# Kernel tuning notes

Measured on AMD Instinct MI355X. Metric: run time of the kernel, lower is better.

The kernel has to match this reference:

```python
import jax, jax.numpy as jnp
import numpy as np

HEAD = 16
NEG = -1.0e9


def setup_inputs() -> dict:
    key = jax.random.key(0)
    ks = jax.random.split(key, 8)
    B, S, D = 2, 2048, 1024
    scale = 1.0 / np.sqrt(D)
    inp = {
        "query": jax.random.normal(ks[0], (B, S, D), jnp.float32),
        "key": jax.random.normal(ks[1], (B, S, D), jnp.float32),
        "value": jax.random.normal(ks[2], (B, S, D), jnp.float32),
        "mask": jnp.ones((B, S, S), jnp.int32),
        "w_q": jax.random.normal(ks[3], (D, D), jnp.float32) * scale,
        "b_q": jnp.zeros((D,), jnp.float32),
        "w_k": jax.random.normal(ks[4], (D, D), jnp.float32) * scale,
        "b_k": jnp.zeros((D,), jnp.float32),
        "w_v": jax.random.normal(ks[5], (D, D), jnp.float32) * scale,
        "b_v": jnp.zeros((D,), jnp.float32),
        "w_o": jax.random.normal(ks[6], (D, D), jnp.float32) * scale,
        "b_o": jnp.zeros((D,), jnp.float32),
    }
    return inp


def _split_heads(x, B, S, H, dk):
    # [B,S,D] -> [B,H,S,dk]
    return x.reshape(B, S, H, dk).transpose(0, 2, 1, 3)


def reference(query, key, value, mask, w_q, b_q, w_k, b_k, w_v, b_v, w_o, b_o):
    B, S, D = query.shape
    H = HEAD
    dk = D // H
    q = _split_heads(query @ w_q.T + b_q, B, S, H, dk)
    k = _split_heads(key @ w_k.T + b_k, B, S, H, dk)
    v = _split_heads(value @ w_v.T + b_v, B, S, H, dk)
    # scores: [B,H,S,S]
    scores = jnp.einsum('bhqd,bhkd->bhqk', q, k) / jnp.sqrt(jnp.float32(dk))
    scores = jnp.where(mask[:, None, :, :] == 0, NEG, scores)
    p = jax.nn.softmax(scores, axis=-1)  # dropout is identity in eval
    x = jnp.einsum('bhqk,bhkd->bhqd', p, v)  # [B,H,S,dk]
    x = x.transpose(0, 2, 1, 3).reshape(B, S, D)
    return x @ w_o.T + b_o
```

## Files before the change

kernel.cpp:

```cpp
#include <hip/hip_runtime.h>

typedef float f32x4 __attribute__((ext_vector_type(4)));
typedef short bf16x8 __attribute__((ext_vector_type(8)));
typedef unsigned short u16x4 __attribute__((ext_vector_type(4)));

#define BB 2
#define SS 2048
#define DM 1024
#define NH 16
#define DKH 64
#define MROWS 4096

__device__ __forceinline__ unsigned short f2bf(float x) {
  union { float f; unsigned int u; } v; v.f = x;
  unsigned int r = v.u + 0x7fffu + ((v.u >> 16) & 1u);
  return (unsigned short)(r >> 16);
}

__device__ __forceinline__ void gll16(const void* g, void* l) {
  __builtin_amdgcn_global_load_lds(
      (const __attribute__((address_space(1))) void*)g,
      (__attribute__((address_space(3))) void*)l, 16, 0, 0);
}

template <int C>
__device__ __forceinline__ float dppf(float x) {
  return __builtin_bit_cast(float,
      __builtin_amdgcn_mov_dpp(__builtin_bit_cast(int, x), C, 0xf, 0xf, true));
}
__device__ __forceinline__ float rowmax16(float v) {
  v = fmaxf(v, dppf<0xB1>(v));
  v = fmaxf(v, dppf<0x4E>(v));
  v = fmaxf(v, dppf<0x141>(v));
  v = fmaxf(v, dppf<0x140>(v));
  return v;
}
__device__ __forceinline__ float rowsum16(float v) {
  v += dppf<0xB1>(v);
  v += dppf<0x4E>(v);
  v += dppf<0x141>(v);
  v += dppf<0x140>(v);
  return v;
}

struct CvtArgs {
  const float* src[7];
  unsigned short* dst[7];
  int n4[7];
};

__global__ __launch_bounds__(256) void cvt7_kernel(CvtArgs a) {
  const int z = blockIdx.y;
  const int i = blockIdx.x * 256 + threadIdx.x;
  if (i >= a.n4[z]) return;
  f32x4 v = ((const f32x4*)a.src[z])[i];
  u16x4 o;
  o[0] = f2bf(v[0]); o[1] = f2bf(v[1]); o[2] = f2bf(v[2]); o[3] = f2bf(v[3]);
  ((u16x4*)a.dst[z])[i] = o;
}

__global__ __launch_bounds__(256) void mask_flags_kernel(const int* __restrict__ mask,
                                                         int* __restrict__ flags) {
  const int bid = blockIdx.x;
  const int b = bid >> 9, qt = (bid >> 4) & 31, kt = bid & 15;
  __shared__ int sf;
  if (threadIdx.x == 0) sf = 0;
  __syncthreads();
  int any0 = 0;
  const size_t base = ((size_t)b * SS + qt * 64) * SS + kt * 128;
  for (int p = 0; p < 32; ++p) {
    int i = p * 256 + threadIdx.x;
    int r = i >> 7, col = i & 127;
    any0 |= (mask[base + (size_t)r * SS + col] == 0);
  }
  if (any0) sf = 1;
  __syncthreads();
  if (threadIdx.x == 0) flags[bid] = sf;
}

struct ProjArgs {
  const unsigned short* A[3];
  const unsigned short* W[3];
  const float* bias[3];
  void* out[3];
  float alpha[3];
  int mode[3];
};

__global__ __launch_bounds__(256, 2) void proj_gemm(ProjArgs args) {
  __shared__ unsigned short As[128][32];
  __shared__ unsigned short Bs[128][32];
  const int z = blockIdx.z;
  const unsigned short* __restrict__ A = args.A[z];
  const unsigned short* __restrict__ W = args.W[z];
  const float* __restrict__ bias = args.bias[z];
  const float alpha = args.alpha[z];
  const int mode = args.mode[z];

  const int tid = threadIdx.x;
  const int w = tid >> 6, lane = tid & 63;
  const int quad = lane >> 4, c = lane & 15;
  const int m0 = blockIdx.x * 128, n0 = blockIdx.y * 128;
  const int wm = (w >> 1) * 64, wn = (w & 1) * 64;
  const int sr = lane >> 2, scc = lane & 3;
  const int lx = scc ^ ((sr >> 1) & 3);
  const int sk = (quad ^ ((c >> 1) & 3)) * 8;

  f32x4 acc[4][4];
#pragma unroll
  for (int i = 0; i < 4; ++i)
#pragma unroll
    for (int j = 0; j < 4; ++j) { f32x4 zz = {0.f, 0.f, 0.f, 0.f}; acc[i][j] = zz; }

  for (int kt = 0; kt < 32; ++kt) {
    const int k0 = kt * 32;
    __syncthreads();
#pragma unroll
    for (int t = 0; t < 2; ++t) {
      const int tt = w + t * 4;
      const int r = tt * 16 + sr;
      gll16(A + (size_t)(m0 + r) * DM + k0 + lx * 8, &As[r][scc * 8]);
      gll16(W + (size_t)(n0 + r) * DM + k0 + lx * 8, &Bs[r][scc * 8]);
    }
    __syncthreads();
    bf16x8 af[4], bfr[4];
#pragma unroll
    for (int i = 0; i < 4; ++i) af[i] = *(const bf16x8*)&As[wm + i * 16 + c][sk];
#pragma unroll
    for (int j = 0; j < 4; ++j) bfr[j] = *(const bf16x8*)&Bs[wn + j * 16 + c][sk];
#pragma unroll
    for (int i = 0; i < 4; ++i)
#pragma unroll
      for (int j = 0; j < 4; ++j)
        acc[i][j] = __builtin_amdgcn_mfma_f32_16x16x32_bf16(af[i], bfr[j], acc[i][j], 0, 0, 0);
  }

#pragma unroll
  for (int i = 0; i < 4; ++i)
#pragma unroll
    for (int j = 0; j < 4; ++j)
#pragma unroll
      for (int r = 0; r < 4; ++r) {
        const int m = m0 + wm + i * 16 + quad * 4 + r;
        const int n = n0 + wn + j * 16 + c;
        const float val = (acc[i][j][r] + bias[n]) * alpha;
        if (mode == 2) {
          ((float*)args.out[z])[(size_t)m * DM + n] = val;
        } else {
          const int bb = m >> 11, s = m & 2047, hh = n >> 6, d = n & 63;
          size_t idx;
          if (mode == 0) {
            idx = (((size_t)(bb * NH + hh)) * SS + s) * DKH + d;
          } else {
            const int sl = s & 127, blk = s >> 7;
            const int jj = sl >> 4, rem = sl & 15, kc = rem >> 2, qd = rem & 3;
            const int pos = kc * 32 + qd * 8 + jj;
            idx = (((size_t)(bb * NH + hh)) * DKH + d) * SS + blk * 128 + pos;
          }
          ((unsigned short*)args.out[z])[idx] = f2bf(val);
        }
      }
}

__global__ __launch_bounds__(256, 3) void attn_kernel(
    const unsigned short* __restrict__ qp, const unsigned short* __restrict__ kp,
    const unsigned short* __restrict__ vtp, const int* __restrict__ mask,
    const int* __restrict__ flags, unsigned short* __restrict__ xb) {
  __shared__ __align__(16) char smem[50176];
  unsigned short (*Ks)[128][32] = (unsigned short (*)[128][32])smem;
  unsigned short (*Vt)[64][32]  = (unsigned short (*)[64][32])(smem + 16384);
  unsigned short (*Qs)[64][32]  = (unsigned short (*)[64][32])(smem + 32768);
  unsigned short (*Ps)[136]     = (unsigned short (*)[136])(smem + 32768);

  const int tid = threadIdx.x;
  const int w = tid >> 6, lane = tid & 63;
  const int quad = lane >> 4, c = lane & 15;
  const int qt = blockIdx.x, bh = blockIdx.y;
  const int b = bh >> 4, h = bh & 15;
  const int q0 = qt * 64;
  const int sr = lane >> 2, scc = lane & 3;
  const int lx = scc ^ ((sr >> 1) & 3);
  const int sk = (quad ^ ((c >> 1) & 3)) * 8;

#pragma unroll
  for (int t = 0; t < 2; ++t) {
    const int tt = w + t * 4;
    const int kk = tt >> 2;
    const int r = (tt & 3) * 16 + sr;
    gll16(qp + ((size_t)bh * SS + q0 + r) * DKH + kk * 32 + lx * 8, &Qs[kk][r][scc * 8]);
  }
  __syncthreads();
  const bf16x8 aq0 = *(const bf16x8*)&Qs[0][w * 16 + c][sk];
  const bf16x8 aq1 = *(const bf16x8*)&Qs[1][w * 16 + c][sk];

  f32x4 acco[4];
#pragma unroll
  for (int j = 0; j < 4; ++j) { f32x4 zz = {0.f, 0.f, 0.f, 0.f}; acco[j] = zz; }
  float m_run[4], l_run[4];
#pragma unroll
  for (int r = 0; r < 4; ++r) { m_run[r] = -3.0e38f; l_run[r] = 0.f; }

  for (int kt = 0; kt < 16; ++kt) {
    const int k0 = kt * 128;
    __syncthreads();
#pragma unroll
    for (int i = 0; i < 4; ++i) {
      const int tt = w * 4 + i;
      {
        const int kk = tt >> 3, r = (tt & 7) * 16 + sr;
        gll16(kp + ((size_t)bh * SS + k0 + r) * DKH + kk * 32 + lx * 8, &Ks[kk][r][scc * 8]);
      }
      {
        const int kc = tt >> 2, d = (tt & 3) * 16 + sr;
        gll16(vtp + ((size_t)bh * DKH + d) * SS + k0 + kc * 32 + lx * 8, &Vt[kc][d][scc * 8]);
      }
    }
    __syncthreads();

    f32x4 accs[8];
#pragma unroll
    for (int j = 0; j < 8; ++j) { f32x4 zz = {0.f, 0.f, 0.f, 0.f}; accs[j] = zz; }
#pragma unroll
    for (int j = 0; j < 8; ++j) {
      const int rowk = j * 16 + c;
      const bf16x8 bk0 = *(const bf16x8*)&Ks[0][rowk][sk];
      const bf16x8 bk1 = *(const bf16x8*)&Ks[1][rowk][sk];
      accs[j] = __builtin_amdgcn_mfma_f32_16x16x32_bf16(aq0, bk0, accs[j], 0, 0, 0);
      accs[j] = __builtin_amdgcn_mfma_f32_16x16x32_bf16(aq1, bk1, accs[j], 0, 0, 0);
    }

    if (flags[((size_t)b * 32 + qt) * 16 + kt]) {
#pragma unroll
      for (int j = 0; j < 8; ++j)
#pragma unroll
        for (int r = 0; r < 4; ++r) {
          const int qq = q0 + w * 16 + quad * 4 + r;
          const int kk2 = k0 + j * 16 + c;
          if (mask[((size_t)b * SS + qq) * SS + kk2] == 0) accs[j][r] = -1.0e30f;
        }
    }

    float al[4];
#pragma unroll
    for (int r = 0; r < 4; ++r) {
      float v = accs[0][r];
#pragma unroll
      for (int j = 1; j < 8; ++j) v = fmaxf(v, accs[j][r]);
      v = rowmax16(v);
      const float mn = fmaxf(m_run[r], v);
      al[r] = __builtin_amdgcn_exp2f(m_run[r] - mn);
      m_run[r] = mn;
      float s = 0.f;
      union { bf16x8 v8; unsigned short u[8]; } pk;
#pragma unroll
      for (int j = 0; j < 8; ++j) {
        const float p = __builtin_amdgcn_exp2f(accs[j][r] - mn);
        union { float f; unsigned int u; } pv; pv.f = p;
        pk.u[j] = (unsigned short)(pv.u >> 16);
        union { unsigned int u; float f; } pr; pr.u = pv.u & 0xffff0000u;
        s += pr.f;
      }
      *(bf16x8*)&Ps[w * 16 + quad * 4 + r][c * 8] = pk.v8;
      s = rowsum16(s);
      l_run[r] = l_run[r] * al[r] + s;
    }
#pragma unroll
    for (int j = 0; j < 4; ++j)
#pragma unroll
      for (int r = 0; r < 4; ++r) acco[j][r] *= al[r];

#pragma unroll
    for (int kc = 0; kc < 4; ++kc) {
      const bf16x8 ap = *(const bf16x8*)&Ps[w * 16 + c][kc * 32 + quad * 8];
#pragma unroll
      for (int j = 0; j < 4; ++j) {
        const bf16x8 bv = *(const bf16x8*)&Vt[kc][j * 16 + c][sk];
        acco[j] = __builtin_amdgcn_mfma_f32_16x16x32_bf16(ap, bv, acco[j], 0, 0, 0);
      }
    }
  }

#pragma unroll
  for (int r = 0; r < 4; ++r) {
    const float inv = 1.0f / l_run[r];
    const int q = q0 + w * 16 + quad * 4 + r;
#pragma unroll
    for (int j = 0; j < 4; ++j) {
      xb[((size_t)b * SS + q) * DM + h * DKH + j * 16 + c] = f2bf(acco[j][r] * inv);
    }
  }
}

extern "C" void kernel_launch(void* const* d_in, const int* in_sizes, int n_in,
                              void* d_out, int out_size, void* d_ws, size_t ws_size,
                              hipStream_t stream) {
  (void)in_sizes; (void)n_in; (void)out_size; (void)ws_size;
  const float* query = (const float*)d_in[0];
  const float* key_  = (const float*)d_in[1];
  const float* value = (const float*)d_in[2];
  const int*   mask  = (const int*)d_in[3];
  const float* w_q = (const float*)d_in[4];
  const float* b_q = (const float*)d_in[5];
  const float* w_k = (const float*)d_in[6];
  const float* b_k = (const float*)d_in[7];
  const float* w_v = (const float*)d_in[8];
  const float* b_v = (const float*)d_in[9];
  const float* w_o = (const float*)d_in[10];
  const float* b_o = (const float*)d_in[11];

  char* ws = (char*)d_ws;
  const size_t SZ_IN = (size_t)MROWS * DM * 2;
  const size_t SZ_W  = (size_t)DM * DM * 2;
  unsigned short* qin = (unsigned short*)(ws);
  unsigned short* kin = (unsigned short*)(ws + SZ_IN);
  unsigned short* vin = (unsigned short*)(ws + 2 * SZ_IN);
  unsigned short* wqb = (unsigned short*)(ws + 3 * SZ_IN);
  unsigned short* wkb = (unsigned short*)(ws + 3 * SZ_IN + SZ_W);
  unsigned short* wvb = (unsigned short*)(ws + 3 * SZ_IN + 2 * SZ_W);
  unsigned short* wob = (unsigned short*)(ws + 3 * SZ_IN + 3 * SZ_W);
  unsigned short* qp  = (unsigned short*)(ws + 3 * SZ_IN + 4 * SZ_W);
  unsigned short* kp  = (unsigned short*)(ws + 4 * SZ_IN + 4 * SZ_W);
  unsigned short* vtp = (unsigned short*)(ws + 5 * SZ_IN + 4 * SZ_W);
  unsigned short* xb  = (unsigned short*)(ws + 6 * SZ_IN + 4 * SZ_W);
  int* flags          = (int*)(ws + 7 * SZ_IN + 4 * SZ_W);

  CvtArgs ca;
  ca.src[0] = query; ca.src[1] = key_; ca.src[2] = value;
  ca.src[3] = w_q; ca.src[4] = w_k; ca.src[5] = w_v; ca.src[6] = w_o;
  ca.dst[0] = qin; ca.dst[1] = kin; ca.dst[2] = vin;
  ca.dst[3] = wqb; ca.dst[4] = wkb; ca.dst[5] = wvb; ca.dst[6] = wob;
  ca.n4[0] = ca.n4[1] = ca.n4[2] = MROWS * DM / 4;
  ca.n4[3] = ca.n4[4] = ca.n4[5] = ca.n4[6] = DM * DM / 4;
  cvt7_kernel<<<dim3(4096, 7), 256, 0, stream>>>(ca);

  mask_flags_kernel<<<dim3(1024), 256, 0, stream>>>(mask, flags);

  ProjArgs pa;
  pa.A[0] = qin; pa.A[1] = kin; pa.A[2] = vin;
  pa.W[0] = wqb; pa.W[1] = wkb; pa.W[2] = wvb;
  pa.bias[0] = b_q; pa.bias[1] = b_k; pa.bias[2] = b_v;
  pa.out[0] = qp; pa.out[1] = kp; pa.out[2] = vtp;
  pa.alpha[0] = 0.18033688011112042f; pa.alpha[1] = 1.f; pa.alpha[2] = 1.f;
  pa.mode[0] = 0; pa.mode[1] = 0; pa.mode[2] = 1;
  proj_gemm<<<dim3(32, 8, 3), 256, 0, stream>>>(pa);

  attn_kernel<<<dim3(32, 32), 256, 0, stream>>>(qp, kp, vtp, mask, flags, xb);

  ProjArgs po;
  po.A[0] = po.A[1] = po.A[2] = xb;
  po.W[0] = po.W[1] = po.W[2] = wob;
  po.bias[0] = po.bias[1] = po.bias[2] = b_o;
  po.out[0] = po.out[1] = po.out[2] = d_out;
  po.alpha[0] = po.alpha[1] = po.alpha[2] = 1.f;
  po.mode[0] = po.mode[1] = po.mode[2] = 2;
  proj_gemm<<<dim3(32, 8, 1), 256, 0, stream>>>(po);
}
```

Baseline: 299.3 us.

## Widen attention query tile to 128 and split-K the output projection with atomics

Each attention block now handles 128 query rows (two 16-row tiles per wave), so every K/V tile loaded into LDS is reused across twice as many queries. The P buffer drops its padding and uses an XOR swizzle instead to avoid LDS bank conflicts. The output projection is split along K into two halves that atomically add into an output pre-filled with the bias, doubling the number of blocks. The trade-off is higher register and LDS pressure in attention, with occupancy lowered to 2 blocks, plus extra atomic traffic and an added init kernel.

```diff
diff --git a/kernel.cpp b/kernel.cpp
--- a/kernel.cpp
+++ b/kernel.cpp
@@ -59,16 +59,22 @@
   ((u16x4*)a.dst[z])[i] = o;
 }
 
+__global__ __launch_bounds__(256) void init_out_kernel(const float* __restrict__ b_o,
+                                                       float* __restrict__ out) {
+  const int i = blockIdx.x * 256 + threadIdx.x;
+  ((f32x4*)out)[i] = ((const f32x4*)b_o)[i & 255];
+}
+
 __global__ __launch_bounds__(256) void mask_flags_kernel(const int* __restrict__ mask,
                                                          int* __restrict__ flags) {
   const int bid = blockIdx.x;
-  const int b = bid >> 9, qt = (bid >> 4) & 31, kt = bid & 15;
+  const int b = bid >> 8, qt = (bid >> 4) & 15, kt = bid & 15;
   __shared__ int sf;
   if (threadIdx.x == 0) sf = 0;
   __syncthreads();
   int any0 = 0;
-  const size_t base = ((size_t)b * SS + qt * 64) * SS + kt * 128;
-  for (int p = 0; p < 32; ++p) {
+  const size_t base = ((size_t)b * SS + qt * 128) * SS + kt * 128;
+  for (int p = 0; p < 64; ++p) {
     int i = p * 256 + threadIdx.x;
     int r = i >> 7, col = i & 127;
     any0 |= (mask[base + (size_t)r * SS + col] == 0);
@@ -85,9 +91,11 @@
   void* out[3];
   float alpha[3];
   int mode[3];
+  int kstart[3];
+  int kcount[3];
 };
 
-__global__ __launch_bounds__(256, 2) void proj_gemm(ProjArgs args) {
+__global__ __launch_bounds__(256, 3) void proj_gemm(ProjArgs args) {
   __shared__ unsigned short As[128][32];
   __shared__ unsigned short Bs[128][32];
   const int z = blockIdx.z;
@@ -96,6 +104,7 @@
   const float* __restrict__ bias = args.bias[z];
   const float alpha = args.alpha[z];
   const int mode = args.mode[z];
+  const int kbeg = args.kstart[z], kend = args.kstart[z] + args.kcount[z];
 
   const int tid = threadIdx.x;
   const int w = tid >> 6, lane = tid & 63;
@@ -112,7 +121,7 @@
 #pragma unroll
     for (int j = 0; j < 4; ++j) { f32x4 zz = {0.f, 0.f, 0.f, 0.f}; acc[i][j] = zz; }
 
-  for (int kt = 0; kt < 32; ++kt) {
+  for (int kt = kbeg; kt < kend; ++kt) {
     const int k0 = kt * 32;
     __syncthreads();
 #pragma unroll
@@ -143,6 +152,10 @@
       for (int r = 0; r < 4; ++r) {
         const int m = m0 + wm + i * 16 + quad * 4 + r;
         const int n = n0 + wn + j * 16 + c;
+        if (mode == 3) {
+          atomicAdd(&((float*)args.out[z])[(size_t)m * DM + n], acc[i][j][r]);
+          continue;
+        }
         const float val = (acc[i][j][r] + bias[n]) * alpha;
         if (mode == 2) {
           ((float*)args.out[z])[(size_t)m * DM + n] = val;
@@ -162,43 +175,51 @@
       }
 }
 
-__global__ __launch_bounds__(256, 3) void attn_kernel(
+__global__ __launch_bounds__(256, 2) void attn_kernel(
     const unsigned short* __restrict__ qp, const unsigned short* __restrict__ kp,
     const unsigned short* __restrict__ vtp, const int* __restrict__ mask,
     const int* __restrict__ flags, unsigned short* __restrict__ xb) {
-  __shared__ __align__(16) char smem[50176];
+  __shared__ __align__(16) char smem[65536];
   unsigned short (*Ks)[128][32] = (unsigned short (*)[128][32])smem;
   unsigned short (*Vt)[64][32]  = (unsigned short (*)[64][32])(smem + 16384);
-  unsigned short (*Qs)[64][32]  = (unsigned short (*)[64][32])(smem + 32768);
-  unsigned short (*Ps)[136]     = (unsigned short (*)[136])(smem + 32768);
+  unsigned short (*Qs)[128][32] = (unsigned short (*)[128][32])(smem + 32768);
+  unsigned short (*Ps)[128]     = (unsigned short (*)[128])(smem + 32768);
 
   const int tid = threadIdx.x;
   const int w = tid >> 6, lane = tid & 63;
   const int quad = lane >> 4, c = lane & 15;
   const int qt = blockIdx.x, bh = blockIdx.y;
   const int b = bh >> 4, h = bh & 15;
-  const int q0 = qt * 64;
+  const int q0 = qt * 128;
   const int sr = lane >> 2, scc = lane & 3;
   const int lx = scc ^ ((sr >> 1) & 3);
   const int sk = (quad ^ ((c >> 1) & 3)) * 8;
 
 #pragma unroll
-  for (int t = 0; t < 2; ++t) {
-    const int tt = w + t * 4;
-    const int kk = tt >> 2;
-    const int r = (tt & 3) * 16 + sr;
+  for (int t = 0; t < 4; ++t) {
+    const int tt = w * 4 + t;
+    const int kk = tt >> 3;
+    const int r = (tt & 7) * 16 + sr;
     gll16(qp + ((size_t)bh * SS + q0 + r) * DKH + kk * 32 + lx * 8, &Qs[kk][r][scc * 8]);
   }
   __syncthreads();
-  const bf16x8 aq0 = *(const bf16x8*)&Qs[0][w * 16 + c][sk];
-  const bf16x8 aq1 = *(const bf16x8*)&Qs[1][w * 16 + c][sk];
-
-  f32x4 acco[4];
-#pragma unroll
-  for (int j = 0; j < 4; ++j) { f32x4 zz = {0.f, 0.f, 0.f, 0.f}; acco[j] = zz; }
-  float m_run[4], l_run[4];
-#pragma unroll
-  for (int r = 0; r < 4; ++r) { m_run[r] = -3.0e38f; l_run[r] = 0.f; }
+  bf16x8 aq[2][2];
+#pragma unroll
+  for (int rt = 0; rt < 2; ++rt)
+#pragma unroll
+    for (int kk = 0; kk < 2; ++kk)
+      aq[rt][kk] = *(const bf16x8*)&Qs[kk][w * 32 + rt * 16 + c][sk];
+
+  f32x4 acco[2][4];
+#pragma unroll
+  for (int rt = 0; rt < 2; ++rt)
+#pragma unroll
+    for (int j = 0; j < 4; ++j) { f32x4 zz = {0.f, 0.f, 0.f, 0.f}; acco[rt][j] = zz; }
+  float m_run[2][4], l_run[2][4];
+#pragma unroll
+  for (int rt = 0; rt < 2; ++rt)
+#pragma unroll
+    for (int r = 0; r < 4; ++r) { m_run[rt][r] = -3.0e38f; l_run[rt][r] = 0.f; }
 
   for (int kt = 0; kt < 16; ++kt) {
     const int k0 = kt * 128;
@@ -217,78 +238,95 @@
     }
     __syncthreads();
 
-    f32x4 accs[8];
-#pragma unroll
-    for (int j = 0; j < 8; ++j) { f32x4 zz = {0.f, 0.f, 0.f, 0.f}; accs[j] = zz; }
+    f32x4 accs[2][8];
+#pragma unroll
+    for (int rt = 0; rt < 2; ++rt)
+#pragma unroll
+      for (int j = 0; j < 8; ++j) { f32x4 zz = {0.f, 0.f, 0.f, 0.f}; accs[rt][j] = zz; }
 #pragma unroll
     for (int j = 0; j < 8; ++j) {
       const int rowk = j * 16 + c;
       const bf16x8 bk0 = *(const bf16x8*)&Ks[0][rowk][sk];
       const bf16x8 bk1 = *(const bf16x8*)&Ks[1][rowk][sk];
-      accs[j] = __builtin_amdgcn_mfma_f32_16x16x32_bf16(aq0, bk0, accs[j], 0, 0, 0);
-      accs[j] = __builtin_amdgcn_mfma_f32_16x16x32_bf16(aq1, bk1, accs[j], 0, 0, 0);
-    }
-
-    if (flags[((size_t)b * 32 + qt) * 16 + kt]) {
-#pragma unroll
-      for (int j = 0; j < 8; ++j)
-#pragma unroll
-        for (int r = 0; r < 4; ++r) {
-          const int qq = q0 + w * 16 + quad * 4 + r;
-          const int kk2 = k0 + j * 16 + c;
-          if (mask[((size_t)b * SS + qq) * SS + kk2] == 0) accs[j][r] = -1.0e30f;
+#pragma unroll
+      for (int rt = 0; rt < 2; ++rt) {
+        accs[rt][j] = __builtin_amdgcn_mfma_f32_16x16x32_bf16(aq[rt][0], bk0, accs[rt][j], 0, 0, 0);
+        accs[rt][j] = __builtin_amdgcn_mfma_f32_16x16x32_bf16(aq[rt][1], bk1, accs[rt][j], 0, 0, 0);
+      }
+    }
+
+    if (flags[((size_t)b * 16 + qt) * 16 + kt]) {
+#pragma unroll
+      for (int rt = 0; rt < 2; ++rt)
+#pragma unroll
+        for (int j = 0; j < 8; ++j)
+#pragma unroll
+          for (int r = 0; r < 4; ++r) {
+            const int qq = q0 + w * 32 + rt * 16 + quad * 4 + r;
+            const int kk2 = k0 + j * 16 + c;
+            if (mask[((size_t)b * SS + qq) * SS + kk2] == 0) accs[rt][j][r] = -1.0e30f;
+          }
+    }
+
+    float al[2][4];
+#pragma unroll
+    for (int rt = 0; rt < 2; ++rt)
+#pragma unroll
+      for (int r = 0; r < 4; ++r) {
+        float v = accs[rt][0][r];
+#pragma unroll
+        for (int j = 1; j < 8; ++j) v = fmaxf(v, accs[rt][j][r]);
+        v = rowmax16(v);
+        const float mn = fmaxf(m_run[rt][r], v);
+        al[rt][r] = __builtin_amdgcn_exp2f(m_run[rt][r] - mn);
+        m_run[rt][r] = mn;
+        float s = 0.f;
+        union { bf16x8 v8; unsigned short u[8]; } pk;
+#pragma unroll
+        for (int j = 0; j < 8; ++j) {
+          const float p = __builtin_amdgcn_exp2f(accs[rt][j][r] - mn);
+          union { float f; unsigned int u; } pv; pv.f = p;
+          pk.u[j] = (unsigned short)(pv.u >> 16);
+          union { unsigned int u; float f; } pr; pr.u = pv.u & 0xffff0000u;
+          s += pr.f;
         }
-    }
-
-    float al[4];
-#pragma unroll
-    for (int r = 0; r < 4; ++r) {
-      float v = accs[0][r];
-#pragma unroll
-      for (int j = 1; j < 8; ++j) v = fmaxf(v, accs[j][r]);
-      v = rowmax16(v);
-      const float mn = fmaxf(m_run[r], v);
-      al[r] = __builtin_amdgcn_exp2f(m_run[r] - mn);
-      m_run[r] = mn;
-      float s = 0.f;
-      union { bf16x8 v8; unsigned short u[8]; } pk;
-#pragma unroll
-      for (int j = 0; j < 8; ++j) {
-        const float p = __builtin_amdgcn_exp2f(accs[j][r] - mn);
-        union { float f; unsigned int u; } pv; pv.f = p;
-        pk.u[j] = (unsigned short)(pv.u >> 16);
-        union { unsigned int u; float f; } pr; pr.u = pv.u & 0xffff0000u;
-        s += pr.f;
-      }
-      *(bf16x8*)&Ps[w * 16 + quad * 4 + r][c * 8] = pk.v8;
-      s = rowsum16(s);
-      l_run[r] = l_run[r] * al[r] + s;
-    }
-#pragma unroll
-    for (int j = 0; j < 4; ++j)
-#pragma unroll
-      for (int r = 0; r < 4; ++r) acco[j][r] *= al[r];
+        const int prow = w * 32 + rt * 16 + quad * 4 + r;
+        *(bf16x8*)&Ps[prow][(c ^ ((prow >> 1) & 7)) * 8] = pk.v8;
+        s = rowsum16(s);
+        l_run[rt][r] = l_run[rt][r] * al[rt][r] + s;
+      }
+#pragma unroll
+    for (int rt = 0; rt < 2; ++rt)
+#pragma unroll
+      for (int j = 0; j < 4; ++j)
+#pragma unroll
+        for (int r = 0; r < 4; ++r) acco[rt][j][r] *= al[rt][r];
 
 #pragma unroll
     for (int kc = 0; kc < 4; ++kc) {
-      const bf16x8 ap = *(const bf16x8*)&Ps[w * 16 + c][kc * 32 + quad * 8];
+      const int pc = ((kc * 4 + quad) ^ ((c >> 1) & 7)) * 8;
+      const bf16x8 ap0 = *(const bf16x8*)&Ps[w * 32 + c][pc];
+      const bf16x8 ap1 = *(const bf16x8*)&Ps[w * 32 + 16 + c][pc];
 #pragma unroll
       for (int j = 0; j < 4; ++j) {
         const bf16x8 bv = *(const bf16x8*)&Vt[kc][j * 16 + c][sk];
-        acco[j] = __builtin_amdgcn_mfma_f32_16x16x32_bf16(ap, bv, acco[j], 0, 0, 0);
+        acco[0][j] = __builtin_amdgcn_mfma_f32_16x16x32_bf16(ap0, bv, acco[0][j], 0, 0, 0);
+        acco[1][j] = __builtin_amdgcn_mfma_f32_16x16x32_bf16(ap1, bv, acco[1][j], 0, 0, 0);
       }
     }
   }
 
 #pragma unroll
-  for (int r = 0; r < 4; ++r) {
-    const float inv = 1.0f / l_run[r];
-    const int q = q0 + w * 16 + quad * 4 + r;
-#pragma unroll
-    for (int j = 0; j < 4; ++j) {
-      xb[((size_t)b * SS + q) * DM + h * DKH + j * 16 + c] = f2bf(acco[j][r] * inv);
-    }
-  }
+  for (int rt = 0; rt < 2; ++rt)
+#pragma unroll
+    for (int r = 0; r < 4; ++r) {
+      const float inv = 1.0f / l_run[rt][r];
+      const int q = q0 + w * 32 + rt * 16 + quad * 4 + r;
+#pragma unroll
+      for (int j = 0; j < 4; ++j) {
+        xb[((size_t)b * SS + q) * DM + h * DKH + j * 16 + c] = f2bf(acco[rt][j][r] * inv);
+      }
+    }
 }
 
 extern "C" void kernel_launch(void* const* d_in, const int* in_sizes, int n_in,
@@ -333,7 +371,9 @@
   ca.n4[3] = ca.n4[4] = ca.n4[5] = ca.n4[6] = DM * DM / 4;
   cvt7_kernel<<<dim3(4096, 7), 256, 0, stream>>>(ca);
 
-  mask_flags_kernel<<<dim3(1024), 256, 0, stream>>>(mask, flags);
+  init_out_kernel<<<dim3(4096), 256, 0, stream>>>(b_o, (float*)d_out);
+
+  mask_flags_kernel<<<dim3(512), 256, 0, stream>>>(mask, flags);
 
   ProjArgs pa;
   pa.A[0] = qin; pa.A[1] = kin; pa.A[2] = vin;
@@ -342,9 +382,11 @@
   pa.out[0] = qp; pa.out[1] = kp; pa.out[2] = vtp;
   pa.alpha[0] = 0.18033688011112042f; pa.alpha[1] = 1.f; pa.alpha[2] = 1.f;
   pa.mode[0] = 0; pa.mode[1] = 0; pa.mode[2] = 1;
+  pa.kstart[0] = pa.kstart[1] = pa.kstart[2] = 0;
+  pa.kcount[0] = pa.kcount[1] = pa.kcount[2] = 32;
   proj_gemm<<<dim3(32, 8, 3), 256, 0, stream>>>(pa);
 
-  attn_kernel<<<dim3(32, 32), 256, 0, stream>>>(qp, kp, vtp, mask, flags, xb);
+  attn_kernel<<<dim3(16, 32), 256, 0, stream>>>(qp, kp, vtp, mask, flags, xb);
 
   ProjArgs po;
   po.A[0] = po.A[1] = po.A[2] = xb;
@@ -352,6 +394,8 @@
   po.bias[0] = po.bias[1] = po.bias[2] = b_o;
   po.out[0] = po.out[1] = po.out[2] = d_out;
   po.alpha[0] = po.alpha[1] = po.alpha[2] = 1.f;
-  po.mode[0] = po.mode[1] = po.mode[2] = 2;
-  proj_gemm<<<dim3(32, 8, 1), 256, 0, stream>>>(po);
-}
+  po.mode[0] = po.mode[1] = po.mode[2] = 3;
+  po.kstart[0] = 0; po.kstart[1] = 16; po.kstart[2] = 0;
+  po.kcount[0] = po.kcount[1] = 16; po.kcount[2] = 32;
+  proj_gemm<<<dim3(32, 8, 2), 256, 0, stream>>>(po);
+}
```

New measurement: 309.8 us. 1.04x slower.
